# Performance work log

Hardware: AMD Instinct MI355X
Metric: run time of the kernel (lower is better)

## Reference

```python
import jax, jax.numpy as jnp
import numpy as np

EMB_DIM = 2048
USER_DIM = 256
NUM_EXPERTS = 64
TOP_K = 8
N_TOKENS = 16384


def setup_inputs() -> dict:
    key = jax.random.key(0)
    k_h, k_u, k_w = jax.random.split(key, 3)
    h = jax.random.normal(k_h, (N_TOKENS, EMB_DIM), dtype=jnp.float32)
    u = jax.random.normal(k_u, (N_TOKENS, USER_DIM), dtype=jnp.float32)
    # nn.Linear weight is [out, in]; we store transposed [in, out] for x @ W
    W = jax.random.normal(k_w, (EMB_DIM + USER_DIM, NUM_EXPERTS), dtype=jnp.float32) * (1.0 / np.sqrt(EMB_DIM + USER_DIM))
    b = jnp.zeros((NUM_EXPERTS,), dtype=jnp.float32)
    return {"h": h, "u": u, "W": W, "b": b}


def reference(h, u, W, b):
    # gate logits: [N, E]
    g = jnp.concatenate([h, u], axis=-1) @ W + b
    w = jax.nn.softmax(g, axis=-1)
    # top-k mask + renormalize (top_k < num_experts)
    _, top_idx = jax.lax.top_k(w, TOP_K)                       # [N, k]
    mask = jax.nn.one_hot(top_idx, NUM_EXPERTS, dtype=w.dtype).sum(axis=-2)  # [N, E]
    w = w * mask
    w = w / (w.sum(axis=-1, keepdims=True) + 1e-9)
    return w
```

## Files before the change

### kernel.cpp

```cpp
#include <hip/hip_runtime.h>

#define EMB 2048
#define UDIM 256
#define KTOT 2304
#define NE 64
#define TOPK 8
#define TPB 16
#define LP 65
#define SSH 6144

typedef __attribute__((ext_vector_type(8))) short short8;
typedef __attribute__((ext_vector_type(4))) float f32x4;
typedef __attribute__((ext_vector_type(4))) unsigned int u32x4;

__device__ __forceinline__ unsigned short bf16h(float x) {
  unsigned uu = __builtin_bit_cast(unsigned, x);
  return (unsigned short)((uu + 0x7FFFu + ((uu >> 16) & 1u)) >> 16);
}
__device__ __forceinline__ float bf2f(unsigned short s) {
  return __builtin_bit_cast(float, ((unsigned)s) << 16);
}

__device__ __forceinline__ unsigned cvtpk(float a, float b) {
  unsigned r;
  asm("v_cvt_pk_bf16_f32 %0, %1, %2" : "=v"(r) : "v"(a), "v"(b));
  return r;
}

__global__ __launch_bounds__(256)
void prep_w(const float* __restrict__ W, unsigned short* __restrict__ wb) {
  const int flat = blockIdx.x * 256 + threadIdx.x;
  const int k = flat >> 6;
  const int n = flat & 63;
  const float w = W[flat];
  const unsigned short h0 = bf16h(w);
  const float r1 = w - bf2f(h0);
  const unsigned short h1 = bf16h(r1);
  const float r2 = r1 - bf2f(h1);
  const unsigned short h2 = bf16h(r2);

  const int s = k >> 5;
  const int kk = k & 31;
  const int lane = (kk >> 3) * 16 + (n & 15);
  const int j = kk & 7;
  const int nt = n >> 4;
  const size_t base = (size_t)s * SSH + ((size_t)nt * 64 + lane) * 8 + j;
  wb[base] = h0;
  wb[base + 2048] = h1;
  wb[base + 4096] = h2;
}

__global__ __launch_bounds__(512, 8)
void gate_mfma(const float* __restrict__ h, const float* __restrict__ u,
               const unsigned short* __restrict__ wb,
               const float* __restrict__ b, float* __restrict__ out) {
  __shared__ float slab[4][TPB * LP];

  const int tid = threadIdx.x;
  const int lane = tid & 63;
  const int kq = __builtin_amdgcn_readfirstlane(tid >> 6);
  const int mm = lane & 15;
  const int q8 = (lane >> 4) * 8;
  const int tok0 = blockIdx.x * TPB;
  const int token = tok0 + mm;

  const float* hrow = h + (size_t)token * EMB + q8;
  const float* urow = u + (size_t)token * UDIM + q8;
  const unsigned short* wlane = wb + (size_t)lane * 8;

  f32x4 acc[4];
#pragma unroll
  for (int nt = 0; nt < 4; ++nt) acc[nt] = 0.f;

  auto run = [&](const float* __restrict__ xp, int kw0, int nsteps) {
    f32x4 c0 = *(const f32x4*)(xp);
    f32x4 c1 = *(const f32x4*)(xp + 4);
    const int as0 = kw0 >> 5;
    for (int s = 0; s < nsteps; ++s) {
      const unsigned short* ws = wlane + (size_t)(as0 + s) * SSH;
      short8 Bv[3][4];
#pragma unroll
      for (int p = 0; p < 3; ++p)
#pragma unroll
        for (int nt = 0; nt < 4; ++nt)
          Bv[p][nt] = *(const short8*)(ws + (p * 4 + nt) * 512);

      f32x4 n0 = 0.f, n1 = 0.f;
      if (s + 1 < nsteps) {
        n0 = *(const f32x4*)(xp + (s + 1) * 32);
        n1 = *(const f32x4*)(xp + (s + 1) * 32 + 4);
      }

      float xs[8] = {c0[0], c0[1], c0[2], c0[3], c1[0], c1[1], c1[2], c1[3]};
      u32x4 W0, W1, W2;
#pragma unroll
      for (int k2 = 0; k2 < 4; ++k2) {
        const float a = xs[2 * k2], bb = xs[2 * k2 + 1];
        const unsigned p0 = cvtpk(a, bb);
        const float a1 = a - __builtin_bit_cast(float, p0 << 16);
        const float b1 = bb - __builtin_bit_cast(float, p0 & 0xFFFF0000u);
        const unsigned p1 = cvtpk(a1, b1);
        const float a2 = a1 - __builtin_bit_cast(float, p1 << 16);
        const float b2 = b1 - __builtin_bit_cast(float, p1 & 0xFFFF0000u);
        const unsigned p2 = cvtpk(a2, b2);
        W0[k2] = p0; W1[k2] = p1; W2[k2] = p2;
      }
      const short8 A0 = __builtin_bit_cast(short8, W0);
      const short8 A1 = __builtin_bit_cast(short8, W1);
      const short8 A2 = __builtin_bit_cast(short8, W2);

#pragma unroll
      for (int nt = 0; nt < 4; ++nt) {
        acc[nt] = __builtin_amdgcn_mfma_f32_16x16x32_bf16(A0, Bv[0][nt], acc[nt], 0, 0, 0);
        acc[nt] = __builtin_amdgcn_mfma_f32_16x16x32_bf16(A0, Bv[1][nt], acc[nt], 0, 0, 0);
        acc[nt] = __builtin_amdgcn_mfma_f32_16x16x32_bf16(A1, Bv[0][nt], acc[nt], 0, 0, 0);
        acc[nt] = __builtin_amdgcn_mfma_f32_16x16x32_bf16(A1, Bv[1][nt], acc[nt], 0, 0, 0);
        acc[nt] = __builtin_amdgcn_mfma_f32_16x16x32_bf16(A0, Bv[2][nt], acc[nt], 0, 0, 0);
        acc[nt] = __builtin_amdgcn_mfma_f32_16x16x32_bf16(A2, Bv[0][nt], acc[nt], 0, 0, 0);
      }
      c0 = n0; c1 = n1;
    }
  };

  if (kq < 7) {
    run(hrow + kq * 288, kq * 288, 9);
  } else {
    run(hrow + 2016, 2016, 1);
    run(urow, 2048, 8);
  }

  const int row = (lane >> 4) * 4;
  const int bsel = kq & 3;
  if (kq < 4) {
#pragma unroll
    for (int nt = 0; nt < 4; ++nt)
#pragma unroll
      for (int r = 0; r < 4; ++r)
        slab[bsel][(row + r) * LP + nt * 16 + mm] = acc[nt][r];
  }
  __syncthreads();
  if (kq >= 4) {
#pragma unroll
    for (int nt = 0; nt < 4; ++nt)
#pragma unroll
      for (int r = 0; r < 4; ++r)
        slab[bsel][(row + r) * LP + nt * 16 + mm] += acc[nt][r];
  }
  __syncthreads();

  const float bias = b[lane];
#pragma unroll
  for (int tt = 0; tt < 2; ++tt) {
    const int t = kq * 2 + tt;
    float g = slab[0][t * LP + lane] + slab[1][t * LP + lane] +
              slab[2][t * LP + lane] + slab[3][t * LP + lane] + bias;

    float m = g;
#pragma unroll
    for (int off = 32; off > 0; off >>= 1)
      m = fmaxf(m, __shfl_xor(m, off));
    float pexp = __expf(g - m);
    float s = pexp;
#pragma unroll
    for (int off = 32; off > 0; off >>= 1)
      s += __shfl_xor(s, off);
    const float pn = pexp / s;

    float vv = pn;
    float topsum = 0.f;
    int sel = 0;
    for (int r = 0; r < TOPK; ++r) {
      float mv = vv;
      int mi = lane;
#pragma unroll
      for (int off = 32; off > 0; off >>= 1) {
        const float ov = __shfl_xor(mv, off);
        const int oi = __shfl_xor(mi, off);
        if (ov > mv || (ov == mv && oi < mi)) { mv = ov; mi = oi; }
      }
      topsum += mv;
      if (lane == mi) { sel = 1; vv = -1.f; }
    }

    out[(size_t)(tok0 + t) * NE + lane] =
        sel ? pn / (topsum + 1e-9f) : 0.f;
  }
}

extern "C" void kernel_launch(void* const* d_in, const int* in_sizes, int n_in,
                              void* d_out, int out_size, void* d_ws, size_t ws_size,
                              hipStream_t stream) {
  const float* h = (const float*)d_in[0];
  const float* u = (const float*)d_in[1];
  const float* W = (const float*)d_in[2];
  const float* b = (const float*)d_in[3];
  float* out = (float*)d_out;

  unsigned short* wb = (unsigned short*)d_ws;

  const int n_tokens = in_sizes[0] / EMB;

  hipLaunchKernelGGL(prep_w, dim3(KTOT * NE / 256), dim3(256), 0, stream, W, wb);
  hipLaunchKernelGGL(gate_mfma, dim3(n_tokens / TPB), dim3(512), 0, stream,
                     h, u, wb, b, out);
}
```

Baseline: 265.1 us.

## Restructure gate GEMM to per-wave token tiles with double-buffered LDS weight staging

Result: slower. 296.3 us (+11.8%).

```diff
diff --git a/kernel.cpp b/kernel.cpp
--- a/kernel.cpp
+++ b/kernel.cpp
@@ -5,9 +5,12 @@
 #define KTOT 2304
 #define NE 64
 #define TOPK 8
-#define TPB 16
 #define LP 65
 #define SSH 6144
+#define STEPB 12288
+#define CH 4
+#define CHB (CH * STEPB)
+#define NCHUNK 18
 
 typedef __attribute__((ext_vector_type(8))) short short8;
 typedef __attribute__((ext_vector_type(4))) float f32x4;
@@ -50,48 +53,64 @@
   wb[base + 4096] = h2;
 }
 
-__global__ __launch_bounds__(512, 8)
+__global__ __launch_bounds__(256, 1)
 void gate_mfma(const float* __restrict__ h, const float* __restrict__ u,
                const unsigned short* __restrict__ wb,
                const float* __restrict__ b, float* __restrict__ out) {
-  __shared__ float slab[4][TPB * LP];
+  __shared__ __align__(1024) char lds[2 * CHB];
 
   const int tid = threadIdx.x;
   const int lane = tid & 63;
-  const int kq = __builtin_amdgcn_readfirstlane(tid >> 6);
+  const int wid = __builtin_amdgcn_readfirstlane(tid >> 6);
   const int mm = lane & 15;
   const int q8 = (lane >> 4) * 8;
-  const int tok0 = blockIdx.x * TPB;
-  const int token = tok0 + mm;
+  const int tok0 = blockIdx.x * 64;
+  const int token = tok0 + wid * 16 + mm;
 
   const float* hrow = h + (size_t)token * EMB + q8;
   const float* urow = u + (size_t)token * UDIM + q8;
-  const unsigned short* wlane = wb + (size_t)lane * 8;
+
+  const char* gsrc0 = (const char*)wb + (size_t)wid * STEPB + (size_t)lane * 16;
 
   f32x4 acc[4];
 #pragma unroll
   for (int nt = 0; nt < 4; ++nt) acc[nt] = 0.f;
 
-  auto run = [&](const float* __restrict__ xp, int kw0, int nsteps) {
-    f32x4 c0 = *(const f32x4*)(xp);
-    f32x4 c1 = *(const f32x4*)(xp + 4);
-    const int as0 = kw0 >> 5;
-    for (int s = 0; s < nsteps; ++s) {
-      const unsigned short* ws = wlane + (size_t)(as0 + s) * SSH;
+  auto stage = [&](int c) {
+    const char* s = gsrc0 + (size_t)c * CHB;
+    char* d = (char*)lds + (size_t)((c & 1) * CHB) + (size_t)wid * STEPB;
+#pragma unroll
+    for (int j = 0; j < 12; ++j)
+      __builtin_amdgcn_global_load_lds(
+          (const __attribute__((address_space(1))) unsigned int*)(s + j * 1024),
+          (__attribute__((address_space(3))) unsigned int*)(d + j * 1024),
+          16, 0, 0);
+  };
+
+  auto aload = [&](int c, f32x4* A) {
+    const float* base = (c < 16) ? (hrow + c * 128) : (urow + (c - 16) * 128);
+#pragma unroll
+    for (int s = 0; s < CH; ++s) {
+      A[2 * s] = *(const f32x4*)(base + s * 32);
+      A[2 * s + 1] = *(const f32x4*)(base + s * 32 + 4);
+    }
+  };
+
+  auto compute = [&](int bufsel, const f32x4* A) {
+    const char* lb = (const char*)lds + bufsel * CHB + (size_t)lane * 16;
+#pragma unroll
+    for (int s = 0; s < CH; ++s) {
+      const short8* ws = (const short8*)(lb + s * STEPB);
       short8 Bv[3][4];
 #pragma unroll
       for (int p = 0; p < 3; ++p)
 #pragma unroll
         for (int nt = 0; nt < 4; ++nt)
-          Bv[p][nt] = *(const short8*)(ws + (p * 4 + nt) * 512);
-
-      f32x4 n0 = 0.f, n1 = 0.f;
-      if (s + 1 < nsteps) {
-        n0 = *(const f32x4*)(xp + (s + 1) * 32);
-        n1 = *(const f32x4*)(xp + (s + 1) * 32 + 4);
-      }
-
-      float xs[8] = {c0[0], c0[1], c0[2], c0[3], c1[0], c1[1], c1[2], c1[3]};
+          Bv[p][nt] = ws[(p * 4 + nt) * 64];
+
+      const f32x4 c0 = A[2 * s], c1 = A[2 * s + 1];
+      const float xs[8] = {c0[0], c0[1], c0[2], c0[3],
+                           c1[0], c1[1], c1[2], c1[3]};
       u32x4 W0, W1, W2;
 #pragma unroll
       for (int k2 = 0; k2 < 4; ++k2) {
@@ -118,42 +137,42 @@
         acc[nt] = __builtin_amdgcn_mfma_f32_16x16x32_bf16(A0, Bv[2][nt], acc[nt], 0, 0, 0);
         acc[nt] = __builtin_amdgcn_mfma_f32_16x16x32_bf16(A2, Bv[0][nt], acc[nt], 0, 0, 0);
       }
-      c0 = n0; c1 = n1;
     }
   };
 
-  if (kq < 7) {
-    run(hrow + kq * 288, kq * 288, 9);
-  } else {
-    run(hrow + 2016, 2016, 1);
-    run(urow, 2048, 8);
+  f32x4 Aa[8], Ab[8];
+  stage(0);
+  aload(0, Aa);
+  __syncthreads();
+
+#pragma unroll 1
+  for (int cc = 0; cc < NCHUNK / 2; ++cc) {
+    const int c0 = 2 * cc;
+    aload(c0 + 1, Ab);
+    stage(c0 + 1);
+    compute(0, Aa);
+    __syncthreads();
+    if (c0 + 2 < NCHUNK) {
+      aload(c0 + 2, Aa);
+      stage(c0 + 2);
+    }
+    compute(1, Ab);
+    __syncthreads();
   }
 
-  const int row = (lane >> 4) * 4;
-  const int bsel = kq & 3;
-  if (kq < 4) {
-#pragma unroll
-    for (int nt = 0; nt < 4; ++nt)
-#pragma unroll
-      for (int r = 0; r < 4; ++r)
-        slab[bsel][(row + r) * LP + nt * 16 + mm] = acc[nt][r];
-  }
+  float* slab = (float*)lds + (size_t)wid * (16 * LP);
+  const int rowb = (lane >> 4) * 4;
+#pragma unroll
+  for (int nt = 0; nt < 4; ++nt)
+#pragma unroll
+    for (int r = 0; r < 4; ++r)
+      slab[(rowb + r) * LP + nt * 16 + mm] = acc[nt][r];
   __syncthreads();
-  if (kq >= 4) {
-#pragma unroll
-    for (int nt = 0; nt < 4; ++nt)
-#pragma unroll
-      for (int r = 0; r < 4; ++r)
-        slab[bsel][(row + r) * LP + nt * 16 + mm] += acc[nt][r];
-  }
-  __syncthreads();
 
   const float bias = b[lane];
-#pragma unroll
-  for (int tt = 0; tt < 2; ++tt) {
-    const int t = kq * 2 + tt;
-    float g = slab[0][t * LP + lane] + slab[1][t * LP + lane] +
-              slab[2][t * LP + lane] + slab[3][t * LP + lane] + bias;
+#pragma unroll 1
+  for (int tt = 0; tt < 16; ++tt) {
+    float g = slab[tt * LP + lane] + bias;
 
     float m = g;
 #pragma unroll
@@ -182,7 +201,7 @@
       if (lane == mi) { sel = 1; vv = -1.f; }
     }
 
-    out[(size_t)(tok0 + t) * NE + lane] =
+    out[(size_t)(tok0 + wid * 16 + tt) * NE + lane] =
         sel ? pn / (topsum + 1e-9f) : 0.f;
   }
 }
@@ -201,6 +220,6 @@
   const int n_tokens = in_sizes[0] / EMB;
 
   hipLaunchKernelGGL(prep_w, dim3(KTOT * NE / 256), dim3(256), 0, stream, W, wb);
-  hipLaunchKernelGGL(gate_mfma, dim3(n_tokens / TPB), dim3(512), 0, stream,
+  hipLaunchKernelGGL(gate_mfma, dim3(n_tokens / 64), dim3(256), 0, stream,
                      h, u, wb, b, out);
 }
```

## Halve waves per block and double-buffer B fragments across K steps

Applied to the files above, without the earlier changes.

After: 253.7 us. 1.05x faster.

```diff
diff --git a/kernel.cpp b/kernel.cpp
--- a/kernel.cpp
+++ b/kernel.cpp
@@ -50,7 +50,7 @@
   wb[base + 4096] = h2;
 }
 
-__global__ __launch_bounds__(512, 8)
+__global__ __launch_bounds__(256, 3)
 void gate_mfma(const float* __restrict__ h, const float* __restrict__ u,
                const unsigned short* __restrict__ wb,
                const float* __restrict__ b, float* __restrict__ out) {
@@ -72,86 +72,84 @@
 #pragma unroll
   for (int nt = 0; nt < 4; ++nt) acc[nt] = 0.f;
 
+  auto body = [&](const f32x4& c0, const f32x4& c1, const short8* Bc) {
+    const float xs[8] = {c0[0], c0[1], c0[2], c0[3],
+                         c1[0], c1[1], c1[2], c1[3]};
+    u32x4 W0, W1, W2;
+#pragma unroll
+    for (int k2 = 0; k2 < 4; ++k2) {
+      const float a = xs[2 * k2], bb = xs[2 * k2 + 1];
+      const unsigned p0 = cvtpk(a, bb);
+      const float a1 = a - __builtin_bit_cast(float, p0 << 16);
+      const float b1 = bb - __builtin_bit_cast(float, p0 & 0xFFFF0000u);
+      const unsigned p1 = cvtpk(a1, b1);
+      const float a2 = a1 - __builtin_bit_cast(float, p1 << 16);
+      const float b2 = b1 - __builtin_bit_cast(float, p1 & 0xFFFF0000u);
+      const unsigned p2 = cvtpk(a2, b2);
+      W0[k2] = p0; W1[k2] = p1; W2[k2] = p2;
+    }
+    const short8 A0 = __builtin_bit_cast(short8, W0);
+    const short8 A1 = __builtin_bit_cast(short8, W1);
+    const short8 A2 = __builtin_bit_cast(short8, W2);
+
+#pragma unroll
+    for (int nt = 0; nt < 4; ++nt) {
+      acc[nt] = __builtin_amdgcn_mfma_f32_16x16x32_bf16(A0, Bc[0 + nt], acc[nt], 0, 0, 0);
+      acc[nt] = __builtin_amdgcn_mfma_f32_16x16x32_bf16(A0, Bc[4 + nt], acc[nt], 0, 0, 0);
+      acc[nt] = __builtin_amdgcn_mfma_f32_16x16x32_bf16(A1, Bc[0 + nt], acc[nt], 0, 0, 0);
+      acc[nt] = __builtin_amdgcn_mfma_f32_16x16x32_bf16(A1, Bc[4 + nt], acc[nt], 0, 0, 0);
+      acc[nt] = __builtin_amdgcn_mfma_f32_16x16x32_bf16(A0, Bc[8 + nt], acc[nt], 0, 0, 0);
+      acc[nt] = __builtin_amdgcn_mfma_f32_16x16x32_bf16(A2, Bc[0 + nt], acc[nt], 0, 0, 0);
+    }
+  };
+
   auto run = [&](const float* __restrict__ xp, int kw0, int nsteps) {
+    const int as0 = kw0 >> 5;
     f32x4 c0 = *(const f32x4*)(xp);
     f32x4 c1 = *(const f32x4*)(xp + 4);
-    const int as0 = kw0 >> 5;
-    for (int s = 0; s < nsteps; ++s) {
-      const unsigned short* ws = wlane + (size_t)(as0 + s) * SSH;
-      short8 Bv[3][4];
-#pragma unroll
-      for (int p = 0; p < 3; ++p)
-#pragma unroll
-        for (int nt = 0; nt < 4; ++nt)
-          Bv[p][nt] = *(const short8*)(ws + (p * 4 + nt) * 512);
-
-      f32x4 n0 = 0.f, n1 = 0.f;
-      if (s + 1 < nsteps) {
-        n0 = *(const f32x4*)(xp + (s + 1) * 32);
-        n1 = *(const f32x4*)(xp + (s + 1) * 32 + 4);
-      }
-
-      float xs[8] = {c0[0], c0[1], c0[2], c0[3], c1[0], c1[1], c1[2], c1[3]};
-      u32x4 W0, W1, W2;
-#pragma unroll
-      for (int k2 = 0; k2 < 4; ++k2) {
-        const float a = xs[2 * k2], bb = xs[2 * k2 + 1];
-        const unsigned p0 = cvtpk(a, bb);
-        const float a1 = a - __builtin_bit_cast(float, p0 << 16);
-        const float b1 = bb - __builtin_bit_cast(float, p0 & 0xFFFF0000u);
-        const unsigned p1 = cvtpk(a1, b1);
-        const float a2 = a1 - __builtin_bit_cast(float, p1 << 16);
-        const float b2 = b1 - __builtin_bit_cast(float, p1 & 0xFFFF0000u);
-        const unsigned p2 = cvtpk(a2, b2);
-        W0[k2] = p0; W1[k2] = p1; W2[k2] = p2;
-      }
-      const short8 A0 = __builtin_bit_cast(short8, W0);
-      const short8 A1 = __builtin_bit_cast(short8, W1);
-      const short8 A2 = __builtin_bit_cast(short8, W2);
-
-#pragma unroll
-      for (int nt = 0; nt < 4; ++nt) {
-        acc[nt] = __builtin_amdgcn_mfma_f32_16x16x32_bf16(A0, Bv[0][nt], acc[nt], 0, 0, 0);
-        acc[nt] = __builtin_amdgcn_mfma_f32_16x16x32_bf16(A0, Bv[1][nt], acc[nt], 0, 0, 0);
-        acc[nt] = __builtin_amdgcn_mfma_f32_16x16x32_bf16(A1, Bv[0][nt], acc[nt], 0, 0, 0);
-        acc[nt] = __builtin_amdgcn_mfma_f32_16x16x32_bf16(A1, Bv[1][nt], acc[nt], 0, 0, 0);
-        acc[nt] = __builtin_amdgcn_mfma_f32_16x16x32_bf16(A0, Bv[2][nt], acc[nt], 0, 0, 0);
-        acc[nt] = __builtin_amdgcn_mfma_f32_16x16x32_bf16(A2, Bv[0][nt], acc[nt], 0, 0, 0);
-      }
+    short8 Bc[12];
+    {
+      const unsigned short* ws = wlane + (size_t)as0 * SSH;
+#pragma unroll
+      for (int q = 0; q < 12; ++q) Bc[q] = *(const short8*)(ws + q * 512);
+    }
+#pragma unroll 1
+    for (int s = 0; s < nsteps - 1; ++s) {
+      const f32x4 n0 = *(const f32x4*)(xp + (s + 1) * 32);
+      const f32x4 n1 = *(const f32x4*)(xp + (s + 1) * 32 + 4);
+      short8 Bn[12];
+      const unsigned short* ws = wlane + (size_t)(as0 + s + 1) * SSH;
+#pragma unroll
+      for (int q = 0; q < 12; ++q) Bn[q] = *(const short8*)(ws + q * 512);
+
+      body(c0, c1, Bc);
+
       c0 = n0; c1 = n1;
-    }
+#pragma unroll
+      for (int q = 0; q < 12; ++q) Bc[q] = Bn[q];
+    }
+    body(c0, c1, Bc);
   };
 
-  if (kq < 7) {
-    run(hrow + kq * 288, kq * 288, 9);
+  if (kq < 3) {
+    run(hrow + kq * 576, kq * 576, 18);
   } else {
-    run(hrow + 2016, 2016, 1);
+    run(hrow + 1728, 1728, 10);
     run(urow, 2048, 8);
   }
 
-  const int row = (lane >> 4) * 4;
-  const int bsel = kq & 3;
-  if (kq < 4) {
-#pragma unroll
-    for (int nt = 0; nt < 4; ++nt)
-#pragma unroll
-      for (int r = 0; r < 4; ++r)
-        slab[bsel][(row + r) * LP + nt * 16 + mm] = acc[nt][r];
-  }
+  const int rowb = (lane >> 4) * 4;
+#pragma unroll
+  for (int nt = 0; nt < 4; ++nt)
+#pragma unroll
+    for (int r = 0; r < 4; ++r)
+      slab[kq][(rowb + r) * LP + nt * 16 + mm] = acc[nt][r];
   __syncthreads();
-  if (kq >= 4) {
-#pragma unroll
-    for (int nt = 0; nt < 4; ++nt)
-#pragma unroll
-      for (int r = 0; r < 4; ++r)
-        slab[bsel][(row + r) * LP + nt * 16 + mm] += acc[nt][r];
-  }
-  __syncthreads();
 
   const float bias = b[lane];
 #pragma unroll
-  for (int tt = 0; tt < 2; ++tt) {
-    const int t = kq * 2 + tt;
+  for (int tt = 0; tt < 4; ++tt) {
+    const int t = kq * 4 + tt;
     float g = slab[0][t * LP + lane] + slab[1][t * LP + lane] +
               slab[2][t * LP + lane] + slab[3][t * LP + lane] + bias;
 
@@ -201,6 +199,6 @@
   const int n_tokens = in_sizes[0] / EMB;
 
   hipLaunchKernelGGL(prep_w, dim3(KTOT * NE / 256), dim3(256), 0, stream, W, wb);
-  hipLaunchKernelGGL(gate_mfma, dim3(n_tokens / TPB), dim3(512), 0, stream,
+  hipLaunchKernelGGL(gate_mfma, dim3(n_tokens / TPB), dim3(256), 0, stream,
                      h, u, wb, b, out);
 }
```
